# Performance work log

Measured on AMD Instinct MI355X. Metric: run time of the kernel, lower is better.

Reference implementation:

```python
import jax, jax.numpy as jnp
import numpy as np

N = 100000   # nodes
E = 1000000  # edges
F_IN = 15    # node feature dim
H = 64       # hidden dim
EMB = 128    # embedding dim
R = 13       # relations
NB = 4       # bases


def _xavier(key, shape):
    fan_in, fan_out = shape[-2], shape[-1]
    lim = float(np.sqrt(6.0 / (fan_in + fan_out)))
    return jax.random.uniform(key, shape, jnp.float32, -lim, lim)


def setup_inputs() -> dict:
    key = jax.random.key(0)
    ks = jax.random.split(key, 24)
    inp = {}
    inp["node_features"] = jax.random.normal(ks[0], (N, F_IN), jnp.float32)
    inp["edge_index"] = jax.random.randint(ks[1], (2, E), 0, N, jnp.int32)
    inp["edge_type"] = jax.random.randint(ks[2], (E,), 0, R, jnp.int32)
    # input projection (15 -> 64)
    inp["W_in"] = _xavier(ks[3], (F_IN, H)); inp["b_in"] = jnp.zeros((H,), jnp.float32)
    # RGCN layer 0
    inp["Wself0"] = _xavier(ks[4], (H, H)); inp["bself0"] = jnp.zeros((H,), jnp.float32)
    inp["bases0"] = _xavier(ks[5], (NB, H, H))
    inp["coeffs0"] = _xavier(ks[6], (R, NB))
    # RGCN layer 1
    inp["Wself1"] = _xavier(ks[7], (H, H)); inp["bself1"] = jnp.zeros((H,), jnp.float32)
    inp["bases1"] = _xavier(ks[8], (NB, H, H))
    inp["coeffs1"] = _xavier(ks[9], (R, NB))
    # readout MLP (2H -> H -> EMB)
    inp["Wr1"] = _xavier(ks[10], (2 * H, H)); inp["br1"] = jnp.zeros((H,), jnp.float32)
    inp["Wr2"] = _xavier(ks[11], (H, EMB)); inp["br2"] = jnp.zeros((EMB,), jnp.float32)
    # node projection (H -> EMB)
    inp["Wnp"] = _xavier(ks[12], (H, EMB)); inp["bnp"] = jnp.zeros((EMB,), jnp.float32)
    return inp


def _rgcn_layer(h, src, tgt, etype, Wself, bself, bases, coeffs):
    # h: (N, H). Sum over relations of per-relation gather+matmul+scatter-add
    # == single scatter over all edges with per-edge relation weight.
    # Basis decomposition: W_r = sum_b coeffs[r,b] * bases[b].
    h_src = h[src]                 # (E, H) gather
    c_e = coeffs[etype]            # (E, NB) per-edge basis coefficients
    msg = jnp.zeros((h_src.shape[0], bases.shape[2]), h.dtype)
    for b in range(bases.shape[0]):  # fixed small loop over NB=4 bases
        msg = msg + c_e[:, b:b + 1] * (h_src @ bases[b])
    agg = jax.ops.segment_sum(msg, tgt, num_segments=h.shape[0])  # (N, H)
    # NOTE: original code computes degree norm but never applies it (dead code),
    # so aggregation is an unnormalized scatter-add, reproduced faithfully here.
    return jax.nn.relu(h @ Wself + bself + agg)  # dropout is identity in eval


def reference(node_features, edge_index, edge_type, W_in, b_in,
              Wself0, bself0, bases0, coeffs0,
              Wself1, bself1, bases1, coeffs1,
              Wr1, br1, Wr2, br2, Wnp, bnp):
    src, tgt = edge_index[0], edge_index[1]
    h = node_features @ W_in + b_in                      # (N, H)
    h = _rgcn_layer(h, src, tgt, edge_type, Wself0, bself0, bases0, coeffs0)
    h = _rgcn_layer(h, src, tgt, edge_type, Wself1, bself1, bases1, coeffs1)
    # graph readout: mean + max pooling over nodes -> MLP
    g = jnp.concatenate([h.mean(axis=0), h.max(axis=0)])  # (2H,)
    graph_emb = jax.nn.relu(g @ Wr1 + br1) @ Wr2 + br2    # (EMB,)
    node_emb = h @ Wnp + bnp                              # (N, EMB)
    return graph_emb, node_emb
```

## Files before the change

### kernel.cpp

```cpp
#include <hip/hip_runtime.h>
#include <hip/hip_bf16.h>

#define NN 100000
#define EE 1000000
#define FIN 15
#define HH 64
#define EMBD 128
#define RR 13
#define NBASE 4
#define NP 391
#define CAP 1700128
#define SENT (15 << 17)

typedef __hip_bfloat16 bf16;
typedef __attribute__((ext_vector_type(8))) short short8;
typedef __attribute__((ext_vector_type(4))) float f32x4;

__device__ __forceinline__ float b2f(bf16 x) { return __bfloat162float(x); }
__device__ __forceinline__ float bcast(float v, int l) {
    return __uint_as_float(__builtin_amdgcn_readlane(__float_as_uint(v), l));
}
__device__ __forceinline__ int bcasti(int v, int l) {
    return (int)__builtin_amdgcn_readlane((unsigned)v, l);
}
__device__ __forceinline__ unsigned short f2bu(float f) {
    bf16 t = __float2bfloat16(f);
    return *reinterpret_cast<unsigned short*>(&t);
}
__device__ __forceinline__ float bu2f(unsigned u) {
    return __uint_as_float(u << 16);
}

__global__ void k_detect(const void* __restrict__ win, int* __restrict__ flag) {
    int tid = threadIdx.x;
    const bf16* p = (const bf16*)win;
    int cnt = 0;
    for (int i = tid; i < FIN * HH; i += 64) {
        float v = b2f(p[i]);
        if (!(fabsf(v) < 0.3f)) cnt++;
    }
#pragma unroll
    for (int off = 32; off > 0; off >>= 1) cnt += __shfl_down(cnt, off, 64);
    if (tid == 0) *flag = (cnt > 40) ? 1 : 0;
}

struct ConvTab {
    const void* in[17];
    int n[17];
    int cum[18];
};

__global__ void k_convert_all(ConvTab tab, float* __restrict__ base,
                              const int* __restrict__ flag) {
    int g = blockIdx.x * 256 + threadIdx.x;
    if (g >= tab.cum[17]) return;
    int t = 0;
#pragma unroll
    for (int i = 0; i < 17; ++i) if (g >= tab.cum[i + 1]) t = i + 1;
    int local = g - tab.cum[t];
    if (local >= tab.n[t]) return;
    float v;
    if (*flag) v = ((const float*)tab.in[t])[local];
    else       v = b2f(((const bf16*)tab.in[t])[local]);
    base[g] = v;
}

__global__ void k_zero(int* __restrict__ a, int n) {
    int i = blockIdx.x * 256 + threadIdx.x;
    if (i < n) a[i] = 0;
}

__global__ void k_fill(int* __restrict__ a, int n, int val) {
    int i = blockIdx.x * 256 + threadIdx.x;
    if (i < n) a[i] = val;
}

__global__ void k_hist(const int* __restrict__ tgt, int* __restrict__ count,
                       int* __restrict__ rank) {
    int e = blockIdx.x * 256 + threadIdx.x;
    if (e >= EE) return;
    rank[e] = atomicAdd(&count[tgt[e]], 1);
}

__global__ void k_scan1(const int* __restrict__ count, int* __restrict__ scanned,
                        int* __restrict__ partials) {
    __shared__ int buf[256];
    int tid = threadIdx.x;
    int i = blockIdx.x * 256 + tid;
    int v = (i < NN) ? ((count[i] + 7) & ~7) : 0;
    buf[tid] = v;
    __syncthreads();
    for (int off = 1; off < 256; off <<= 1) {
        int t = (tid >= off) ? buf[tid - off] : 0;
        __syncthreads();
        buf[tid] += t;
        __syncthreads();
    }
    if (i < NN) scanned[i] = buf[tid] - v;
    if (tid == 255) partials[blockIdx.x] = buf[255];
}

__global__ void k_scan2(int* __restrict__ partials) {
    __shared__ int buf[512];
    int tid = threadIdx.x;
    int v = (tid < NP) ? partials[tid] : 0;
    buf[tid] = v;
    __syncthreads();
    for (int off = 1; off < 512; off <<= 1) {
        int t = (tid >= off) ? buf[tid - off] : 0;
        __syncthreads();
        buf[tid] += t;
        __syncthreads();
    }
    if (tid < NP) partials[tid] = buf[tid] - v;
}

__global__ void k_scatter(const int* __restrict__ src, const int* __restrict__ tgt,
                          const int* __restrict__ et, const int* __restrict__ rank,
                          const int* __restrict__ scanned, const int* __restrict__ partials,
                          int* __restrict__ packed) {
    int e = blockIdx.x * 256 + threadIdx.x;
    if (e >= EE) return;
    int t = tgt[e];
    int pos = scanned[t] + partials[t >> 8] + rank[e];
    packed[pos] = src[e] | (et[e] << 17);
}

__global__ void k_coef(const float* __restrict__ c0, const float* __restrict__ c1,
                       float* __restrict__ o0, float* __restrict__ o1) {
    int t = threadIdx.x;
    int r = t >> 2, b = t & 3;
    o0[t] = (r < RR) ? c0[r * NBASE + b] : 0.f;
    o1[t] = (r < RR) ? c1[r * NBASE + b] : 0.f;
}

__global__ void k_wcat(const float* __restrict__ bases0, const float* __restrict__ Wself0,
                       const float* __restrict__ bases1, const float* __restrict__ Wself1,
                       unsigned short* __restrict__ W0, unsigned short* __restrict__ W1) {
    int idx = blockIdx.x * 256 + threadIdx.x;
    if (idx >= HH * 320) return;
    int n = idx / 320, k = idx - n * 320;
    int b = k >> 6, kk = k & 63;
    float v0 = (b < 4) ? bases0[b * 4096 + kk * 64 + n] : Wself0[kk * 64 + n];
    float v1 = (b < 4) ? bases1[b * 4096 + kk * 64 + n] : Wself1[kk * 64 + n];
    W0[idx] = f2bu(v0);
    W1[idx] = f2bu(v1);
}

__global__ void k_wt(const float* __restrict__ Wnp, unsigned short* __restrict__ WT) {
    int idx = blockIdx.x * 256 + threadIdx.x;
    if (idx >= EMBD * HH) return;
    int c = idx >> 6, k = idx & 63;
    float w = Wnp[k * EMBD + c];
    unsigned short hi = f2bu(w);
    WT[idx] = hi;
    WT[EMBD * HH + idx] = f2bu(w - bu2f(hi));
}


__global__ void k_input_proj(const float* __restrict__ nf, const float* __restrict__ Win,
                             const float* __restrict__ bin, unsigned short* __restrict__ h) {
    __shared__ float w[FIN * HH];
    __shared__ float bb[HH];
    int tid = threadIdx.x;
    for (int i = tid; i < FIN * HH; i += 256) w[i] = Win[i];
    if (tid < HH) bb[tid] = bin[tid];
    __syncthreads();
    int idx = blockIdx.x * 256 + tid;
    if (idx >= NN * HH) return;
    int n = idx >> 6, j = idx & 63;
    float acc = bb[j];
    const float* row = nf + n * FIN;
#pragma unroll
    for (int k = 0; k < FIN; ++k) acc = fmaf(row[k], w[k * HH + j], acc);
    h[idx] = f2bu(acc);
}

__device__ __forceinline__ void edge_group16(const unsigned short* __restrict__ hin,
                                             const float* __restrict__ cc,
                                             int lane, int pk, int j, float S[4]) {
    float hv[16];
    int rr[16];
#pragma unroll
    for (int k = 0; k < 16; ++k) {
        int v = bcasti(pk, j + k);
        rr[k] = (v >> 17) & 0xF;
        hv[k] = bu2f((unsigned)hin[(v & 0x1FFFF) * HH + lane]);
    }
#pragma unroll
    for (int hh = 0; hh < 2; ++hh) {
        float4 cv[8];
#pragma unroll
        for (int k = 0; k < 8; ++k)
            cv[k] = *(const float4*)(cc + rr[hh * 8 + k] * 4);
#pragma unroll
        for (int k = 0; k < 8; ++k) {
            float hk = hv[hh * 8 + k];
            S[0] = fmaf(cv[k].x, hk, S[0]);
            S[1] = fmaf(cv[k].y, hk, S[1]);
            S[2] = fmaf(cv[k].z, hk, S[2]);
            S[3] = fmaf(cv[k].w, hk, S[3]);
        }
    }
}

__device__ __forceinline__ void edge_group8(const unsigned short* __restrict__ hin,
                                            const float* __restrict__ cc,
                                            int lane, int pk, int j, float S[4]) {
    float hv[8];
    int rr[8];
#pragma unroll
    for (int k = 0; k < 8; ++k) {
        int v = bcasti(pk, j + k);
        rr[k] = (v >> 17) & 0xF;
        hv[k] = bu2f((unsigned)hin[(v & 0x1FFFF) * HH + lane]);
    }
    float4 cv[8];
#pragma unroll
    for (int k = 0; k < 8; ++k) cv[k] = *(const float4*)(cc + rr[k] * 4);
#pragma unroll
    for (int k = 0; k < 8; ++k) {
        float hk = hv[k];
        S[0] = fmaf(cv[k].x, hk, S[0]);
        S[1] = fmaf(cv[k].y, hk, S[1]);
        S[2] = fmaf(cv[k].z, hk, S[2]);
        S[3] = fmaf(cv[k].w, hk, S[3]);
    }
}

__device__ __forceinline__ void gather_node(const unsigned short* __restrict__ hin,
                                            const int* __restrict__ packed,
                                            const float* __restrict__ cc,
                                            int lane, int pk, int s0, int cntp,
                                            float S[4]) {
    int lim = min(64, cntp);
    int j = 0;
    for (; j + 16 <= lim; j += 16) edge_group16(hin, cc, lane, pk, j, S);
    if (j < lim) edge_group8(hin, cc, lane, pk, j, S);
    for (int base = 64; base < cntp; base += 64) {
        int pkx = packed[s0 + base + lane];
        int lim2 = min(64, cntp - base);
        int j2 = 0;
        for (; j2 + 16 <= lim2; j2 += 16) edge_group16(hin, cc, lane, pkx, j2, S);
        if (j2 < lim2) edge_group8(hin, cc, lane, pkx, j2, S);
    }
}

__global__ void __launch_bounds__(256, 6)
k_layer(const unsigned short* __restrict__ hin, const int* __restrict__ packed,
        const int* __restrict__ count, const int* __restrict__ scanned,
        const int* __restrict__ partials, const float* __restrict__ cc,
        const unsigned short* __restrict__ Wc, const float* __restrict__ bself,
        unsigned short* __restrict__ hout) {
    __shared__ __align__(16) unsigned short Sb[16 * 264];
    int tid = threadIdx.x;
    int lane = tid & 63;
    int wv = tid >> 6;
    int t0 = blockIdx.x * 16;
    int nb = t0 + wv * 4;

    int4 c4  = *(const int4*)(count + nb);
    int4 sc4 = *(const int4*)(scanned + nb);
    int pb = partials[t0 >> 8];
    int s00 = sc4.x + pb, s01 = sc4.y + pb, s02 = sc4.z + pb, s03 = sc4.w + pb;
    int cp0 = (c4.x + 7) & ~7, cp1 = (c4.y + 7) & ~7;
    int cp2 = (c4.z + 7) & ~7, cp3 = (c4.w + 7) & ~7;

    int pk0 = packed[s00 + lane];
    int pk1 = packed[s01 + lane];
    int pk2 = packed[s02 + lane];
    int pk3 = packed[s03 + lane];

    float S0[4] = {0, 0, 0, 0}, S1[4] = {0, 0, 0, 0};
    float S2[4] = {0, 0, 0, 0}, S3[4] = {0, 0, 0, 0};
    gather_node(hin, packed, cc, lane, pk0, s00, cp0, S0);
    gather_node(hin, packed, cc, lane, pk1, s01, cp1, S1);
    gather_node(hin, packed, cc, lane, pk2, s02, cp2, S2);
    gather_node(hin, packed, cc, lane, pk3, s03, cp3, S3);

#pragma unroll
    for (int b = 0; b < NBASE; ++b) {
        Sb[(wv * 4 + 0) * 264 + b * 64 + lane] = f2bu(S0[b]);
        Sb[(wv * 4 + 1) * 264 + b * 64 + lane] = f2bu(S1[b]);
        Sb[(wv * 4 + 2) * 264 + b * 64 + lane] = f2bu(S2[b]);
        Sb[(wv * 4 + 3) * 264 + b * 64 + lane] = f2bu(S3[b]);
    }
    __syncthreads();

    int m16 = lane & 15;
    int g = lane >> 4;
    f32x4 acc = {0.f, 0.f, 0.f, 0.f};
    const unsigned short* brow = Wc + (wv * 16 + m16) * 320 + g * 8;
#pragma unroll
    for (int kb = 0; kb < 8; ++kb) {
        short8 a = *(const short8*)(&Sb[m16 * 264 + kb * 32 + g * 8]);
        short8 b = *(const short8*)(brow + kb * 32);
        acc = __builtin_amdgcn_mfma_f32_16x16x32_bf16(a, b, acc, 0, 0, 0);
    }
    const unsigned short* hrow = hin + (t0 + m16) * HH + g * 8;
#pragma unroll
    for (int kb = 0; kb < 2; ++kb) {
        short8 a = *(const short8*)(hrow + kb * 32);
        short8 b = *(const short8*)(brow + 256 + kb * 32);
        acc = __builtin_amdgcn_mfma_f32_16x16x32_bf16(a, b, acc, 0, 0, 0);
    }
    int col = wv * 16 + m16;
    float bias = bself[col];
#pragma unroll
    for (int r = 0; r < 4; ++r) {
        int row = g * 4 + r;
        hout[(t0 + row) * HH + col] = f2bu(fmaxf(acc[r] + bias, 0.f));
    }
}

__global__ void k_reduce(const unsigned short* __restrict__ h, float* __restrict__ psum,
                         float* __restrict__ pmax) {
    __shared__ float ls[256], lm[256];
    int tid = threadIdx.x;
    int j = tid & 63;
    int slot = tid >> 6;
    float s = 0.f, m = -1e30f;
    for (int n = blockIdx.x * 4 + slot; n < NN; n += gridDim.x * 4) {
        float v = bu2f((unsigned)h[n * HH + j]);
        s += v;
        m = fmaxf(m, v);
    }
    ls[tid] = s; lm[tid] = m;
    __syncthreads();
    if (tid < 64) {
        s = ls[tid] + ls[tid + 64] + ls[tid + 128] + ls[tid + 192];
        m = fmaxf(fmaxf(lm[tid], lm[tid + 64]), fmaxf(lm[tid + 128], lm[tid + 192]));
        psum[blockIdx.x * 64 + tid] = s;
        pmax[blockIdx.x * 64 + tid] = m;
    }
}

__global__ void k_finish(const float* __restrict__ psum, const float* __restrict__ pmax,
                         const float* __restrict__ Wr1, const float* __restrict__ br1,
                         const float* __restrict__ Wr2, const float* __restrict__ br2,
                         void* __restrict__ out, const int* __restrict__ flag) {
    __shared__ float ls[256], lm[256];
    __shared__ float g[2 * HH];
    __shared__ float tbuf[HH];
    int tid = threadIdx.x;
    int j = tid & 63;
    int slot = tid >> 6;
    float s = 0.f, m = -1e30f;
    for (int i = slot; i < 256; i += 4) {
        s += psum[i * 64 + j];
        m = fmaxf(m, pmax[i * 64 + j]);
    }
    ls[tid] = s; lm[tid] = m;
    __syncthreads();
    if (tid < 64) {
        s = ls[tid] + ls[tid + 64] + ls[tid + 128] + ls[tid + 192];
        m = fmaxf(fmaxf(lm[tid], lm[tid + 64]), fmaxf(lm[tid + 128], lm[tid + 192]));
        g[tid] = s * (1.0f / NN);
        g[64 + tid] = m;
    }
    __syncthreads();
    if (tid < 64) {
        float acc = br1[tid];
#pragma unroll 8
        for (int k = 0; k < 2 * HH; ++k) acc = fmaf(g[k], Wr1[k * HH + tid], acc);
        tbuf[tid] = fmaxf(acc, 0.f);
    }
    __syncthreads();
    if (tid < EMBD) {
        float acc = br2[tid];
#pragma unroll 8
        for (int k = 0; k < HH; ++k) acc = fmaf(tbuf[k], Wr2[k * EMBD + tid], acc);
        if (*flag) ((float*)out)[tid] = acc;
        else       ((bf16*)out)[tid] = __float2bfloat16(acc);
    }
}

__global__ void __launch_bounds__(256, 8)
k_node_emb2(const unsigned short* __restrict__ h, const unsigned short* __restrict__ WT,
            const float* __restrict__ bnp, void* __restrict__ out,
            const int* __restrict__ flag) {
    int tid = threadIdx.x;
    int lane = tid & 63;
    int wv = tid >> 6;
    int n0 = blockIdx.x * 16;
    int m16 = lane & 15, g = lane >> 4;

    const unsigned short* arow = h + (n0 + m16) * HH + g * 8;
    short8 a0 = *(const short8*)(arow);
    short8 a1 = *(const short8*)(arow + 32);

    int c0 = wv * 32;
    const unsigned short* bp0 = WT + (c0 + m16) * HH + g * 8;
    const unsigned short* bp1 = WT + (c0 + 16 + m16) * HH + g * 8;
    const unsigned short* lp0 = bp0 + EMBD * HH;
    const unsigned short* lp1 = bp1 + EMBD * HH;

    f32x4 accA = {0.f, 0.f, 0.f, 0.f}, accB = {0.f, 0.f, 0.f, 0.f};
    accA = __builtin_amdgcn_mfma_f32_16x16x32_bf16(a0, *(const short8*)bp0, accA, 0, 0, 0);
    accA = __builtin_amdgcn_mfma_f32_16x16x32_bf16(a1, *(const short8*)(bp0 + 32), accA, 0, 0, 0);
    accA = __builtin_amdgcn_mfma_f32_16x16x32_bf16(a0, *(const short8*)lp0, accA, 0, 0, 0);
    accA = __builtin_amdgcn_mfma_f32_16x16x32_bf16(a1, *(const short8*)(lp0 + 32), accA, 0, 0, 0);
    accB = __builtin_amdgcn_mfma_f32_16x16x32_bf16(a0, *(const short8*)bp1, accB, 0, 0, 0);
    accB = __builtin_amdgcn_mfma_f32_16x16x32_bf16(a1, *(const short8*)(bp1 + 32), accB, 0, 0, 0);
    accB = __builtin_amdgcn_mfma_f32_16x16x32_bf16(a0, *(const short8*)lp1, accB, 0, 0, 0);
    accB = __builtin_amdgcn_mfma_f32_16x16x32_bf16(a1, *(const short8*)(lp1 + 32), accB, 0, 0, 0);

    float biasA = bnp[c0 + m16], biasB = bnp[c0 + 16 + m16];
    if (*flag) {
        float* o = (float*)out + EMBD;
#pragma unroll
        for (int r = 0; r < 4; ++r) {
            long node = n0 + g * 4 + r;
            o[node * EMBD + c0 + m16]      = accA[r] + biasA;
            o[node * EMBD + c0 + 16 + m16] = accB[r] + biasB;
        }
    } else {
        bf16* o = (bf16*)out + EMBD;
#pragma unroll
        for (int r = 0; r < 4; ++r) {
            long node = n0 + g * 4 + r;
            o[node * EMBD + c0 + m16]      = __float2bfloat16(accA[r] + biasA);
            o[node * EMBD + c0 + 16 + m16] = __float2bfloat16(accB[r] + biasB);
        }
    }
}

extern "C" void kernel_launch(void* const* d_in, const int* in_sizes, int n_in,
                              void* d_out, int out_size, void* d_ws, size_t ws_size,
                              hipStream_t stream) {
    const int* eidx  = (const int*)d_in[1];
    const int* etype = (const int*)d_in[2];
    const int* src = eidx;
    const int* tgt = eidx + EE;

    int* flag = (int*)d_ws;
    float* base = (float*)d_ws + 16;

    const int fidx[17] = {0, 3, 4, 5, 6, 7, 8, 9, 10, 11, 12, 13, 14, 15, 16, 17, 18};
    ConvTab tab;
    float* conv[19];
    int cum = 0;
    for (int t = 0; t < 17; ++t) {
        int i = fidx[t];
        tab.in[t] = d_in[i];
        tab.n[t] = in_sizes[i];
        tab.cum[t] = cum;
        conv[i] = base + cum;
        cum += (in_sizes[i] + 15) & ~15;
    }
    tab.cum[17] = cum;

    k_detect<<<1, 64, 0, stream>>>(d_in[3], flag);
    k_convert_all<<<(cum + 255) / 256, 256, 0, stream>>>(tab, base, flag);

    float* p = base + cum;
    float* psum = p;  p += 256 * 64;
    float* pmax = p;  p += 256 * 64;
    float* c16a = p;  p += 64;
    float* c16b = p;  p += 64;
    int* count    = (int*)p;           p += NN;
    int* scanned  = (int*)p;           p += NN;
    int* partials = (int*)p;           p += 512;
    int* rank     = (int*)p;           p += EE;
    int* packed   = (int*)p;           p += CAP;
    unsigned short* hbf0 = (unsigned short*)p;
    unsigned short* hbf1 = hbf0 + (size_t)NN * HH;
    unsigned short* Wc0  = hbf1 + (size_t)NN * HH;
    unsigned short* Wc1  = Wc0 + HH * 320;
    unsigned short* WT   = Wc1 + HH * 320;

    const float* nf      = conv[0];
    const float* Win     = conv[3];
    const float* bin     = conv[4];
    const float* Wself0  = conv[5];
    const float* bself0  = conv[6];
    const float* bases0  = conv[7];
    const float* coeffs0 = conv[8];
    const float* Wself1  = conv[9];
    const float* bself1  = conv[10];
    const float* bases1  = conv[11];
    const float* coeffs1 = conv[12];
    const float* Wr1     = conv[13];
    const float* br1     = conv[14];
    const float* Wr2     = conv[15];
    const float* br2     = conv[16];
    const float* Wnp     = conv[17];
    const float* bnp     = conv[18];

    const int NHB = (NN * HH) / 256;
    const int LYB = NN / 16;
    const int EB  = (EE + 255) / 256;

    k_zero<<<(NN + 255) / 256, 256, 0, stream>>>(count, NN);
    k_fill<<<(CAP + 255) / 256, 256, 0, stream>>>(packed, CAP, SENT);
    k_hist<<<EB, 256, 0, stream>>>(tgt, count, rank);
    k_scan1<<<NP, 256, 0, stream>>>(count, scanned, partials);
    k_scan2<<<1, 512, 0, stream>>>(partials);
    k_scatter<<<EB, 256, 0, stream>>>(src, tgt, etype, rank, scanned, partials, packed);

    k_coef<<<1, 64, 0, stream>>>(coeffs0, coeffs1, c16a, c16b);
    k_wcat<<<(HH * 320 + 255) / 256, 256, 0, stream>>>(bases0, Wself0, bases1, Wself1, Wc0, Wc1);
    k_wt<<<(EMBD * HH + 255) / 256, 256, 0, stream>>>(Wnp, WT);
    k_input_proj<<<NHB, 256, 0, stream>>>(nf, Win, bin, hbf0);

    k_layer<<<LYB, 256, 0, stream>>>(hbf0, packed, count, scanned, partials, c16a, Wc0, bself0, hbf1);
    k_layer<<<LYB, 256, 0, stream>>>(hbf1, packed, count, scanned, partials, c16b, Wc1, bself1, hbf0);

    k_reduce<<<256, 256, 0, stream>>>(hbf0, psum, pmax);
    k_finish<<<1, 256, 0, stream>>>(psum, pmax, Wr1, br1, Wr2, br2, d_out, flag);
    k_node_emb2<<<LYB, 256, 0, stream>>>(hbf0, WT, bnp, d_out, flag);
}
```

Measured before the change: 425.2 us.

## Merge setup kernels, replace rank array with second atomic pass, nontemporal gathers

Merges the zero and fill kernels into one init kernel, and merges the coefficient, weight-concat and transpose prep kernels into one prep kernel, which cuts launch count. The per-edge rank array is dropped: the scatter pass now takes slots with a second atomicAdd on a per-node counter, trading a 4MB write and read for extra atomics and a nondeterministic order of edges within each node. The neighbor feature gathers in the layer kernel now use nontemporal loads, which may change how those reads are cached.

```diff
diff --git a/kernel.cpp b/kernel.cpp
--- a/kernel.cpp
+++ b/kernel.cpp
@@ -65,21 +65,18 @@
     base[g] = v;
 }
 
-__global__ void k_zero(int* __restrict__ a, int n) {
+__global__ void k_init(int* __restrict__ count, int* __restrict__ rcnt,
+                       int* __restrict__ packed) {
     int i = blockIdx.x * 256 + threadIdx.x;
-    if (i < n) a[i] = 0;
-}
-
-__global__ void k_fill(int* __restrict__ a, int n, int val) {
-    int i = blockIdx.x * 256 + threadIdx.x;
-    if (i < n) a[i] = val;
-}
-
-__global__ void k_hist(const int* __restrict__ tgt, int* __restrict__ count,
-                       int* __restrict__ rank) {
+    if (i < NN) count[i] = 0;
+    else if (i < 2 * NN) rcnt[i - NN] = 0;
+    else if (i < 2 * NN + CAP) packed[i - 2 * NN] = SENT;
+}
+
+__global__ void k_hist(const int* __restrict__ tgt, int* __restrict__ count) {
     int e = blockIdx.x * 256 + threadIdx.x;
     if (e >= EE) return;
-    rank[e] = atomicAdd(&count[tgt[e]], 1);
+    atomicAdd(&count[tgt[e]], 1);
 }
 
 __global__ void k_scan1(const int* __restrict__ count, int* __restrict__ scanned,
@@ -116,45 +113,50 @@
 }
 
 __global__ void k_scatter(const int* __restrict__ src, const int* __restrict__ tgt,
-                          const int* __restrict__ et, const int* __restrict__ rank,
+                          const int* __restrict__ et,
                           const int* __restrict__ scanned, const int* __restrict__ partials,
-                          int* __restrict__ packed) {
+                          int* __restrict__ rcnt, int* __restrict__ packed) {
     int e = blockIdx.x * 256 + threadIdx.x;
     if (e >= EE) return;
     int t = tgt[e];
-    int pos = scanned[t] + partials[t >> 8] + rank[e];
+    int r = atomicAdd(&rcnt[t], 1);
+    int pos = scanned[t] + partials[t >> 8] + r;
     packed[pos] = src[e] | (et[e] << 17);
 }
 
-__global__ void k_coef(const float* __restrict__ c0, const float* __restrict__ c1,
-                       float* __restrict__ o0, float* __restrict__ o1) {
-    int t = threadIdx.x;
-    int r = t >> 2, b = t & 3;
-    o0[t] = (r < RR) ? c0[r * NBASE + b] : 0.f;
-    o1[t] = (r < RR) ? c1[r * NBASE + b] : 0.f;
-}
-
-__global__ void k_wcat(const float* __restrict__ bases0, const float* __restrict__ Wself0,
+#define PREP_WCAT (HH * 320)
+#define PREP_WT   (EMBD * HH)
+__global__ void k_prep(const float* __restrict__ c0, const float* __restrict__ c1,
+                       float* __restrict__ o0, float* __restrict__ o1,
+                       const float* __restrict__ bases0, const float* __restrict__ Wself0,
                        const float* __restrict__ bases1, const float* __restrict__ Wself1,
-                       unsigned short* __restrict__ W0, unsigned short* __restrict__ W1) {
+                       unsigned short* __restrict__ W0, unsigned short* __restrict__ W1,
+                       const float* __restrict__ Wnp, unsigned short* __restrict__ WT) {
     int idx = blockIdx.x * 256 + threadIdx.x;
-    if (idx >= HH * 320) return;
-    int n = idx / 320, k = idx - n * 320;
-    int b = k >> 6, kk = k & 63;
-    float v0 = (b < 4) ? bases0[b * 4096 + kk * 64 + n] : Wself0[kk * 64 + n];
-    float v1 = (b < 4) ? bases1[b * 4096 + kk * 64 + n] : Wself1[kk * 64 + n];
-    W0[idx] = f2bu(v0);
-    W1[idx] = f2bu(v1);
-}
-
-__global__ void k_wt(const float* __restrict__ Wnp, unsigned short* __restrict__ WT) {
-    int idx = blockIdx.x * 256 + threadIdx.x;
-    if (idx >= EMBD * HH) return;
-    int c = idx >> 6, k = idx & 63;
-    float w = Wnp[k * EMBD + c];
-    unsigned short hi = f2bu(w);
-    WT[idx] = hi;
-    WT[EMBD * HH + idx] = f2bu(w - bu2f(hi));
+    if (idx < 64) {
+        int r = idx >> 2, b = idx & 3;
+        o0[idx] = (r < RR) ? c0[r * NBASE + b] : 0.f;
+        o1[idx] = (r < RR) ? c1[r * NBASE + b] : 0.f;
+        return;
+    }
+    idx -= 64;
+    if (idx < PREP_WCAT) {
+        int n = idx / 320, k = idx - n * 320;
+        int b = k >> 6, kk = k & 63;
+        float v0 = (b < 4) ? bases0[b * 4096 + kk * 64 + n] : Wself0[kk * 64 + n];
+        float v1 = (b < 4) ? bases1[b * 4096 + kk * 64 + n] : Wself1[kk * 64 + n];
+        W0[idx] = f2bu(v0);
+        W1[idx] = f2bu(v1);
+        return;
+    }
+    idx -= PREP_WCAT;
+    if (idx < PREP_WT) {
+        int c = idx >> 6, k = idx & 63;
+        float w = Wnp[k * EMBD + c];
+        unsigned short hi = f2bu(w);
+        WT[idx] = hi;
+        WT[PREP_WT + idx] = f2bu(w - bu2f(hi));
+    }
 }
 
 
@@ -185,7 +187,8 @@
     for (int k = 0; k < 16; ++k) {
         int v = bcasti(pk, j + k);
         rr[k] = (v >> 17) & 0xF;
-        hv[k] = bu2f((unsigned)hin[(v & 0x1FFFF) * HH + lane]);
+        unsigned short us = __builtin_nontemporal_load(hin + (v & 0x1FFFF) * HH + lane);
+        hv[k] = bu2f((unsigned)us);
     }
 #pragma unroll
     for (int hh = 0; hh < 2; ++hh) {
@@ -213,7 +216,8 @@
     for (int k = 0; k < 8; ++k) {
         int v = bcasti(pk, j + k);
         rr[k] = (v >> 17) & 0xF;
-        hv[k] = bu2f((unsigned)hin[(v & 0x1FFFF) * HH + lane]);
+        unsigned short us = __builtin_nontemporal_load(hin + (v & 0x1FFFF) * HH + lane);
+        hv[k] = bu2f((unsigned)us);
     }
     float4 cv[8];
 #pragma unroll
@@ -461,7 +465,7 @@
     int* count    = (int*)p;           p += NN;
     int* scanned  = (int*)p;           p += NN;
     int* partials = (int*)p;           p += 512;
-    int* rank     = (int*)p;           p += EE;
+    int* rcnt     = (int*)p;           p += NN;
     int* packed   = (int*)p;           p += CAP;
     unsigned short* hbf0 = (unsigned short*)p;
     unsigned short* hbf1 = hbf0 + (size_t)NN * HH;
@@ -490,17 +494,17 @@
     const int NHB = (NN * HH) / 256;
     const int LYB = NN / 16;
     const int EB  = (EE + 255) / 256;
-
-    k_zero<<<(NN + 255) / 256, 256, 0, stream>>>(count, NN);
-    k_fill<<<(CAP + 255) / 256, 256, 0, stream>>>(packed, CAP, SENT);
-    k_hist<<<EB, 256, 0, stream>>>(tgt, count, rank);
+    const int IB  = (2 * NN + CAP + 255) / 256;
+    const int PB  = (64 + PREP_WCAT + PREP_WT + 255) / 256;
+
+    k_init<<<IB, 256, 0, stream>>>(count, rcnt, packed);
+    k_hist<<<EB, 256, 0, stream>>>(tgt, count);
     k_scan1<<<NP, 256, 0, stream>>>(count, scanned, partials);
     k_scan2<<<1, 512, 0, stream>>>(partials);
-    k_scatter<<<EB, 256, 0, stream>>>(src, tgt, etype, rank, scanned, partials, packed);
-
-    k_coef<<<1, 64, 0, stream>>>(coeffs0, coeffs1, c16a, c16b);
-    k_wcat<<<(HH * 320 + 255) / 256, 256, 0, stream>>>(bases0, Wself0, bases1, Wself1, Wc0, Wc1);
-    k_wt<<<(EMBD * HH + 255) / 256, 256, 0, stream>>>(Wnp, WT);
+    k_scatter<<<EB, 256, 0, stream>>>(src, tgt, etype, scanned, partials, rcnt, packed);
+
+    k_prep<<<PB, 256, 0, stream>>>(coeffs0, coeffs1, c16a, c16b,
+                                   bases0, Wself0, bases1, Wself1, Wc0, Wc1, Wnp, WT);
     k_input_proj<<<NHB, 256, 0, stream>>>(nf, Win, bin, hbf0);
 
     k_layer<<<LYB, 256, 0, stream>>>(hbf0, packed, count, scanned, partials, c16a, Wc0, bself0, hbf1);
```

Measured after the change: 482.3 us. +13.4%, slower.
